# Kernel optimization log

Hardware: AMD Instinct MI355X
Metric: run time of the kernel (lower is better)

The kernel has to match this reference:

```python
import math
import jax, jax.numpy as jnp
import numpy as np


def _shapley_tables(L):
    """Static subset-lattice tables for L views.

    masks: [M, L] 0/1 membership of view l in subset m (M = 2^L).
    coef:  [L, M] Shapley combination coefficients so that
           shapley[l] = sum_m coef[l, m] * relu(Linear(sum_{j in m} feats[j])).
    Derivation (faithful to the torch loops): for view i and every nonempty
    subset S not containing i, contrib = f(sum_{S u {i}}) - f(feats_i) with
    weight |S|! (L-|S|-1)! / L!, plus f(feats_i)/L.  Letting T = S u {i}
    (|T| >= 2, i in T) and noting sum of weights over all S is (L-1)/L and
    f(feats_i) = f(sum over singleton {i}):
      coef[i, T]          = (|T|-1)! (L-|T|)! / L!   for |T|>=2, i in T
      coef[i, {i}]       += -(L-1)/L + 1/L = -(L-2)/L
    """
    M = 1 << L
    fact = math.factorial
    masks = np.zeros((M, L), np.float32)
    coef = np.zeros((L, M), np.float32)
    for m in range(M):
        bits = [i for i in range(L) if (m >> i) & 1]
        for i in bits:
            masks[m, i] = 1.0
        t = len(bits)
        if t >= 2:
            wgt = fact(t - 1) * fact(L - t) / fact(L)
            for i in bits:
                coef[i, m] += wgt
    for i in range(L):
        coef[i, 1 << i] += -(L - 2) / L
    return jnp.asarray(masks), jnp.asarray(coef)


def setup_inputs() -> dict:
    key = jax.random.key(0)
    k1, k2 = jax.random.split(key)
    L, C, H, W = 5, 64, 128, 256
    feats = jax.random.normal(k1, (L, C, H, W), dtype=jnp.float32)
    w = jax.random.normal(k2, (C, 1), dtype=jnp.float32) / np.sqrt(C)
    b = jnp.zeros((1,), dtype=jnp.float32)
    return {"feats": feats, "w": w, "b": b}


def reference(feats, w, b):
    L, C, H, W = feats.shape
    N = H * W
    masks, coef = _shapley_tables(L)
    x = feats.reshape(L, C, N).transpose(0, 2, 1)          # [L, N, C]
    # all 2^L subset sums in one GEMM over the (tiny) L axis
    subset_sums = jnp.einsum('ml,lnc->mnc', masks, x)       # [M, N, C]
    f_sums = jax.nn.relu(subset_sums @ w + b)               # [M, N, 1]
    shapley = jnp.einsum('lm,mnj->lnj', coef, f_sums)       # [L, N, 1]
    attn = jax.nn.softmax(shapley, axis=0)                  # softmax over views
    fused = jnp.sum(x * attn, axis=0)                       # [N, C]
    return fused.T.reshape(C, H, W)
```

## Files before the change

### kernel.cpp

```cpp
#include <hip/hip_runtime.h>


constexpr int L_VIEWS = 5;
constexpr int C_CH    = 64;
constexpr int NPIX    = 128 * 256;

__global__ __launch_bounds__(256)
void shapley_fusion_kernel(const float* __restrict__ feats,
                           const float* __restrict__ w,
                           const float* __restrict__ bptr,
                           float* __restrict__ out)
{
    const int tid  = threadIdx.x;
    const int h    = tid >> 6;
    const int lane = tid & 63;
    const int q    = lane & 7;
    const int g    = (lane >> 3) & 7;
    const int win  = blockIdx.x * 32;
    const int nq   = win + q * 4;
    const int cA   = h * 8 + g;
    const int cB   = cA + 32;

    const float w0   = w[cA];
    const float w1   = w[cB];
    const float bias = bptr[0];

    float4 va[L_VIEWS][2];
#pragma unroll
    for (int l = 0; l < L_VIEWS; ++l) {
        va[l][0] = *reinterpret_cast<const float4*>(
            feats + ((size_t)(l * C_CH + cA) * NPIX + nq));
        va[l][1] = *reinterpret_cast<const float4*>(
            feats + ((size_t)(l * C_CH + cB) * NPIX + nq));
    }

    float d[L_VIEWS][4];
#pragma unroll
    for (int l = 0; l < L_VIEWS; ++l) {
        d[l][0] = va[l][0].x * w0 + va[l][1].x * w1;
        d[l][1] = va[l][0].y * w0 + va[l][1].y * w1;
        d[l][2] = va[l][0].z * w0 + va[l][1].z * w1;
        d[l][3] = va[l][0].w * w0 + va[l][1].w * w1;
    }

#pragma unroll
    for (int l = 0; l < L_VIEWS; ++l) {
#pragma unroll
        for (int j = 0; j < 4; ++j) {
            d[l][j] += __shfl_xor(d[l][j], 8, 64);
            d[l][j] += __shfl_xor(d[l][j], 16, 64);
            d[l][j] += __shfl_xor(d[l][j], 32, 64);
        }
    }

    __shared__ float4 xl[4][8][L_VIEWS];
    if (g == 0) {
#pragma unroll
        for (int l = 0; l < L_VIEWS; ++l) {
            float4 t; t.x = d[l][0]; t.y = d[l][1]; t.z = d[l][2]; t.w = d[l][3];
            xl[h][q][l] = t;
        }
    }
    __syncthreads();

    const int jm = g & 3;
    const float* xf = reinterpret_cast<const float*>(xl);
    float dm[L_VIEWS];
#pragma unroll
    for (int l = 0; l < L_VIEWS; ++l) {
        float s = 0.f;
#pragma unroll
        for (int hh = 0; hh < 4; ++hh)
            s += xf[(((hh * 8 + q) * L_VIEWS) + l) * 4 + jm];
        dm[l] = s;
    }

    constexpr float WT1 = -0.6f;
    constexpr float WT2 = 0.05f;
    constexpr float WT3 = 1.0f / 30.0f;
    constexpr float WT4 = 0.05f;
    constexpr float WT5 = 0.2f;

    float s[32];
    s[0] = bias;
    float sh[L_VIEWS] = {0.f, 0.f, 0.f, 0.f, 0.f};
#pragma unroll
    for (int m = 1; m < 32; ++m) {
        const int lb  = m & (-m);
        const int lbi = __builtin_ctz(m);
        s[m] = s[m ^ lb] + dm[lbi];
        const float f = fmaxf(s[m], 0.f);
        const int pc = __builtin_popcount(m);
        const float wt = (pc == 1) ? WT1 : (pc == 2) ? WT2
                       : (pc == 3) ? WT3 : (pc == 4) ? WT4 : WT5;
#pragma unroll
        for (int i = 0; i < L_VIEWS; ++i)
            if (m & (1 << i)) sh[i] += wt * f;
    }
    float mx = sh[0];
#pragma unroll
    for (int i = 1; i < L_VIEWS; ++i) mx = fmaxf(mx, sh[i]);
    float e[L_VIEWS];
    float sum = 0.f;
#pragma unroll
    for (int i = 0; i < L_VIEWS; ++i) { e[i] = __expf(sh[i] - mx); sum += e[i]; }
    const float inv = 1.f / sum;
    float attn_mine[L_VIEWS];
#pragma unroll
    for (int i = 0; i < L_VIEWS; ++i) attn_mine[i] = e[i] * inv;

    float attn[L_VIEWS][4];
#pragma unroll
    for (int l = 0; l < L_VIEWS; ++l)
#pragma unroll
        for (int j = 0; j < 4; ++j)
            attn[l][j] = __shfl(attn_mine[l], q + 8 * j, 64);

#pragma unroll
    for (int k = 0; k < 2; ++k) {
        const int c = (k == 0) ? cA : cB;
        float4 acc;
        acc.x = va[0][k].x * attn[0][0];
        acc.y = va[0][k].y * attn[0][1];
        acc.z = va[0][k].z * attn[0][2];
        acc.w = va[0][k].w * attn[0][3];
#pragma unroll
        for (int l = 1; l < L_VIEWS; ++l) {
            acc.x += va[l][k].x * attn[l][0];
            acc.y += va[l][k].y * attn[l][1];
            acc.z += va[l][k].z * attn[l][2];
            acc.w += va[l][k].w * attn[l][3];
        }
        *reinterpret_cast<float4*>(out + (size_t)c * NPIX + nq) = acc;
    }
}

extern "C" void kernel_launch(void* const* d_in, const int* in_sizes, int n_in,
                              void* d_out, int out_size, void* d_ws, size_t ws_size,
                              hipStream_t stream) {
    const float* feats = (const float*)d_in[0];
    const float* w     = (const float*)d_in[1];
    const float* b     = (const float*)d_in[2];
    float* out         = (float*)d_out;

    shapley_fusion_kernel<<<NPIX / 32, 256, 0, stream>>>(feats, w, b, out);
}
```

Before: 15.65 us.

## Use Gray-code subset walk, nontemporal output stores, and occupancy hint

Replaces the 32-entry subset-sum array with a single running sum walked in Gray-code order, which cuts register pressure in the per-pixel Shapley loop. Output stores become nontemporal vector stores so the write-once result does not pollute the cache. Launch bounds now request a minimum of 4 blocks per CU. The Gray-code walk uses additions and subtractions, so floating-point rounding may differ slightly from the original sums.

```diff
diff --git a/kernel.cpp b/kernel.cpp
--- a/kernel.cpp
+++ b/kernel.cpp
@@ -5,7 +5,9 @@
 constexpr int C_CH    = 64;
 constexpr int NPIX    = 128 * 256;
 
-__global__ __launch_bounds__(256)
+typedef float floatx4 __attribute__((ext_vector_type(4)));
+
+__global__ __launch_bounds__(256, 4)
 void shapley_fusion_kernel(const float* __restrict__ feats,
                            const float* __restrict__ w,
                            const float* __restrict__ bptr,
@@ -75,28 +77,23 @@
         dm[l] = s;
     }
 
-    constexpr float WT1 = -0.6f;
-    constexpr float WT2 = 0.05f;
-    constexpr float WT3 = 1.0f / 30.0f;
-    constexpr float WT4 = 0.05f;
-    constexpr float WT5 = 0.2f;
+    constexpr float WTS[6] = {0.f, -0.6f, 0.05f, 1.0f / 30.0f, 0.05f, 0.2f};
 
-    float s[32];
-    s[0] = bias;
+    float S = bias;
     float sh[L_VIEWS] = {0.f, 0.f, 0.f, 0.f, 0.f};
 #pragma unroll
-    for (int m = 1; m < 32; ++m) {
-        const int lb  = m & (-m);
-        const int lbi = __builtin_ctz(m);
-        s[m] = s[m ^ lb] + dm[lbi];
-        const float f = fmaxf(s[m], 0.f);
-        const int pc = __builtin_popcount(m);
-        const float wt = (pc == 1) ? WT1 : (pc == 2) ? WT2
-                       : (pc == 3) ? WT3 : (pc == 4) ? WT4 : WT5;
+    for (int t = 1; t < 32; ++t) {
+        const int gm   = t ^ (t >> 1);
+        const int bit  = __builtin_ctz(t);
+        const bool add = (gm >> bit) & 1;
+        S = add ? (S + dm[bit]) : (S - dm[bit]);
+        const float f  = fmaxf(S, 0.f);
+        const float wt = WTS[__builtin_popcount(gm)];
 #pragma unroll
         for (int i = 0; i < L_VIEWS; ++i)
-            if (m & (1 << i)) sh[i] += wt * f;
+            if (gm & (1 << i)) sh[i] += wt * f;
     }
+
     float mx = sh[0];
 #pragma unroll
     for (int i = 1; i < L_VIEWS; ++i) mx = fmaxf(mx, sh[i]);
@@ -119,7 +116,7 @@
 #pragma unroll
     for (int k = 0; k < 2; ++k) {
         const int c = (k == 0) ? cA : cB;
-        float4 acc;
+        floatx4 acc;
         acc.x = va[0][k].x * attn[0][0];
         acc.y = va[0][k].y * attn[0][1];
         acc.z = va[0][k].z * attn[0][2];
@@ -131,7 +128,8 @@
             acc.z += va[l][k].z * attn[l][2];
             acc.w += va[l][k].w * attn[l][3];
         }
-        *reinterpret_cast<float4*>(out + (size_t)c * NPIX + nq) = acc;
+        __builtin_nontemporal_store(acc,
+            reinterpret_cast<floatx4*>(out + (size_t)c * NPIX + nq));
     }
 }
 
```

Result: no change. 15.59 us (-0.4%).
